# Optimization experiments

Hardware: AMD Instinct MI355X
Metric: run time of the kernel (lower is better)

Reference implementation:

```python
import jax, jax.numpy as jnp
import numpy as np

RADIUS = 12
SIGMA = 5.0
USM_LO, USM_HI = 0.0, 5.0
BEGIN = 0  # cfg.usm_begin_param


def _gauss_kernel_2d():
    x = jnp.arange(-RADIUS, RADIUS + 1, dtype=jnp.float32)
    k = jnp.exp(-0.5 * (x / SIGMA) ** 2)
    k = k / k.sum()
    return jnp.outer(k, k)  # [25, 25]


def setup_inputs() -> dict:
    key = jax.random.key(0)
    k1, k2 = jax.random.split(key)
    img = jax.random.uniform(k1, (16, 3, 512, 512), dtype=jnp.float32)
    features = jax.random.normal(k2, (16, 8), dtype=jnp.float32)
    return {"img": img, "features": features}


def reference(img, features):
    p = features[:, BEGIN:BEGIN + 1]                       # [B, 1]
    param = (jnp.tanh(p) * 0.5 + 0.5) * (USM_HI - USM_LO) + USM_LO

    # depthwise 25x25 gaussian blur with reflect padding
    kernel = jnp.broadcast_to(_gauss_kernel_2d(), (3, 1, 25, 25))  # OIHW, groups=3
    padded = jnp.pad(img, ((0, 0), (0, 0), (RADIUS, RADIUS), (RADIUS, RADIUS)),
                     mode='reflect')
    blurred = jax.lax.conv_general_dilated(
        padded, kernel, window_strides=(1, 1), padding='VALID',
        dimension_numbers=('NCHW', 'OIHW', 'NCHW'), feature_group_count=3)

    out = img + param.reshape(-1, 1, 1, 1) * (img - blurred)
    return out, param
```

## Files before the change

### kernel.cpp

```cpp
#include <hip/hip_runtime.h>
#include <hip/hip_fp16.h>


#define RADIUS 12
#define KS     25
#define TILE   64
#define PT     88
#define TA_LD  104
#define TB_LD  72
#define IMG_W  512
#define IMG_H  512
#define PLANE  (IMG_W * IMG_H)
#define NPLANE 48

#define N_STAGE (PT * 11)

__device__ __constant__ float GW[KS] = {
    0.00453456f, 0.00718308f, 0.01093238f, 0.01598625f, 0.02245983f,
    0.03031760f, 0.03931982f, 0.04899550f, 0.05865827f, 0.06747307f,
    0.07456928f, 0.07918039f, 0.08077993f, 0.07918039f, 0.07456928f,
    0.06747307f, 0.05865827f, 0.04899550f, 0.03931982f, 0.03031760f,
    0.02245983f, 0.01598625f, 0.01093238f, 0.00718308f, 0.00453456f
};

__device__ __forceinline__ int reflect512(int i) {
    i = (i < 0) ? -i : i;
    return (i >= 512) ? (1022 - i) : i;
}

typedef _Float16 h2_t __attribute__((ext_vector_type(2)));

__device__ __forceinline__ unsigned h2u(__half2 h) {
    union { __half2 h; unsigned u; } x; x.h = h; return x.u;
}
__device__ __forceinline__ __half2 u2h(unsigned u) {
    union { unsigned u; __half2 h; } x; x.u = u; return x.h;
}
__device__ __forceinline__ float u_lo(unsigned u) {
    return __half2float(__low2half(u2h(u)));
}
__device__ __forceinline__ float u_hi(unsigned u) {
    return __half2float(__high2half(u2h(u)));
}

#if __has_builtin(__builtin_amdgcn_fdot2)
__device__ __forceinline__ float fdot2u(unsigned a, unsigned b, float c) {
    union { unsigned u; h2_t h; } ua, ub;
    ua.u = a; ub.u = b;
    return __builtin_amdgcn_fdot2(ua.h, ub.h, c, false);
}
#else
__device__ __forceinline__ float fdot2u(unsigned a, unsigned b, float c) {
    return c + u_lo(a) * u_lo(b) + u_hi(a) * u_hi(b);
}
#endif

__global__ __launch_bounds__(256) void usm_fused_kernel(
    const float* __restrict__ img, const float* __restrict__ feat,
    float* __restrict__ out, float* __restrict__ out_param)
{
    __shared__ __half tileA[PT][TA_LD];
    __shared__ __half tmpB[PT][TB_LD];

    const int bid  = blockIdx.x + 8 * blockIdx.y + 64 * blockIdx.z;
    const int swz  = (bid & 7) * 384 + (bid >> 3);
    const int bx   = swz & 7;
    const int by   = (swz >> 3) & 7;
    const int zc   = swz >> 6;

    const int tid = threadIdx.x;
    const int tx0 = bx * TILE, ty0 = by * TILE;
    const int b   = zc / 3;
    const float* __restrict__ src = img + (size_t)zc * PLANE;

    float4 sva[4], svb[4];
#pragma unroll
    for (int it = 0; it < 4; ++it) {
        const int li = tid + it * 256;
        if (it < 3 || li < N_STAGE) {
            const int py = li / 11, s = li - py * 11;
            const int gy = reflect512(ty0 - RADIUS + py);
            const float* __restrict__ rowp = src + (size_t)gy * IMG_W;
            const int gx = tx0 - RADIUS + s * 8;
            if (gx >= 0 && gx + 7 <= 511) {
                sva[it] = *(const float4*)(rowp + gx);
                svb[it] = *(const float4*)(rowp + gx + 4);
            } else {
                float4 va, vb;
                va.x = rowp[reflect512(gx)];     va.y = rowp[reflect512(gx + 1)];
                va.z = rowp[reflect512(gx + 2)]; va.w = rowp[reflect512(gx + 3)];
                vb.x = rowp[reflect512(gx + 4)]; vb.y = rowp[reflect512(gx + 5)];
                vb.z = rowp[reflect512(gx + 6)]; vb.w = rowp[reflect512(gx + 7)];
                sva[it] = va; svb[it] = vb;
            }
        }
    }

    unsigned W2[12];
#pragma unroll
    for (int m = 0; m < 12; ++m)
        W2[m] = h2u(__floats2half2_rn(GW[2 * m], GW[2 * m + 1]));
    const unsigned WE = h2u(__floats2half2_rn(GW[24], 0.f));
    const unsigned WO = h2u(__floats2half2_rn(0.f, GW[24]));

    __half2 GWh2[KS];
#pragma unroll
    for (int k = 0; k < KS; ++k)
        GWh2[k] = __floats2half2_rn(GW[k], GW[k]);

    const float param = (tanhf(feat[b * 8]) * 0.5f + 0.5f) * 5.0f;

#pragma unroll
    for (int it = 0; it < 4; ++it) {
        const int li = tid + it * 256;
        if (it < 3 || li < N_STAGE) {
            const int py = li / 11, s = li - py * 11;
            uint4 pk;
            pk.x = h2u(__floats2half2_rn(sva[it].x, sva[it].y));
            pk.y = h2u(__floats2half2_rn(sva[it].z, sva[it].w));
            pk.z = h2u(__floats2half2_rn(svb[it].x, svb[it].y));
            pk.w = h2u(__floats2half2_rn(svb[it].z, svb[it].w));
            *(uint4*)&tileA[py][s * 8] = pk;
        }
    }
    __syncthreads();

#pragma unroll
    for (int it = 0; it < 3; ++it) {
        const int li = tid + it * 256;
        if (it < 2 || li < PT * (TILE / 8)) {
            const int py = li >> 3, g = li & 7;
            const uint4 qa = *(const uint4*)&tileA[py][g * 8];
            const uint4 qb = *(const uint4*)&tileA[py][g * 8 + 8];
            const uint4 qc = *(const uint4*)&tileA[py][g * 8 + 16];
            const uint4 qd = *(const uint4*)&tileA[py][g * 8 + 24];

            unsigned P[16] = { qa.x, qa.y, qa.z, qa.w, qb.x, qb.y, qb.z, qb.w,
                               qc.x, qc.y, qc.z, qc.w, qd.x, qd.y, qd.z, qd.w };
            unsigned S[15];
#pragma unroll
            for (int i = 0; i < 15; ++i)
                S[i] = __builtin_amdgcn_alignbit(P[i + 1], P[i], 16);

            float acc[8];
#pragma unroll
            for (int h = 0; h < 4; ++h) {
                float a = 0.f;
#pragma unroll
                for (int m = 0; m < 12; ++m) a = fdot2u(P[h + m], W2[m], a);
                acc[2 * h] = fdot2u(P[h + 12], WE, a);
            }
#pragma unroll
            for (int h = 0; h < 4; ++h) {
                float a = 0.f;
#pragma unroll
                for (int m = 0; m < 12; ++m) a = fdot2u(S[h + m], W2[m], a);
                acc[2 * h + 1] = fdot2u(P[h + 12], WO, a);
            }

            uint4 pk;
            pk.x = h2u(__floats2half2_rn(acc[0], acc[1]));
            pk.y = h2u(__floats2half2_rn(acc[2], acc[3]));
            pk.z = h2u(__floats2half2_rn(acc[4], acc[5]));
            pk.w = h2u(__floats2half2_rn(acc[6], acc[7]));
            *(uint4*)&tmpB[py][g * 8] = pk;
        }
    }
    __syncthreads();

    const int tx4 = (tid & 15) * 4, ry0 = (tid >> 4) * 4;

    __half2 aP0[4], aP1[4];
#pragma unroll
    for (int d = 0; d < 4; ++d) { aP0[d] = __half2(0, 0); aP1[d] = __half2(0, 0); }

#pragma unroll
    for (int k = 0; k < KS + 3; ++k) {
        const uint2 rd = *(const uint2*)&tmpB[ry0 + k][tx4];
        const __half2 p0 = u2h(rd.x), p1 = u2h(rd.y);
#pragma unroll
        for (int d = 0; d < 4; ++d) {
            const int kk = k - d;
            if (kk >= 0 && kk < KS) {
                aP0[d] = __hfma2(GWh2[kk], p0, aP0[d]);
                aP1[d] = __hfma2(GWh2[kk], p1, aP1[d]);
            }
        }
    }

    float* __restrict__ dst = out + (size_t)zc * PLANE;
#pragma unroll
    for (int d = 0; d < 4; ++d) {
        const int oy = ty0 + ry0 + d;
        const uint2 cv = *(const uint2*)&tileA[ry0 + d + RADIUS][tx4 + RADIUS];
        const float v0 = u_lo(cv.x), v1 = u_hi(cv.x), v2 = u_lo(cv.y), v3 = u_hi(cv.y);
        const float b0 = __half2float(__low2half(aP0[d])), b1 = __half2float(__high2half(aP0[d]));
        const float b2 = __half2float(__low2half(aP1[d])), b3 = __half2float(__high2half(aP1[d]));
        float4 o;
        o.x = v0 + param * (v0 - b0);
        o.y = v1 + param * (v1 - b1);
        o.z = v2 + param * (v2 - b2);
        o.w = v3 + param * (v3 - b3);
        *(float4*)(dst + (size_t)oy * IMG_W + tx0 + tx4) = o;
    }

    if (tid == 0 && bx == 0 && by == 0 && (zc - b * 3) == 0)
        out_param[b] = param;
}

extern "C" void kernel_launch(void* const* d_in, const int* in_sizes, int n_in,
                              void* d_out, int out_size, void* d_ws, size_t ws_size,
                              hipStream_t stream) {
    const float* img  = (const float*)d_in[0];
    const float* feat = (const float*)d_in[1];
    float* out       = (float*)d_out;
    float* out_param = (float*)d_out + (size_t)NPLANE * PLANE;

    usm_fused_kernel<<<dim3(8, 8, NPLANE), 256, 0, stream>>>(img, feat, out, out_param);
}
```

Baseline: 34.79 us.

## Offload part of horizontal blur pass to MFMA banded-matrix multiply

Computes the horizontal 25-tap blur for the first 48 tile rows with 16x16x32 f16 MFMA instructions against a banded Gaussian weight matrix built in registers. The remaining 40 rows stay on the existing fdot2 VALU path, so matrix and vector units can work concurrently. This reduces VALU pressure in the horizontal pass at the cost of extra registers and MFMAs that multiply many zero band entries. It also relies on the MFMA operand and result lane layouts being mapped correctly.

```diff
diff --git a/kernel.cpp b/kernel.cpp
--- a/kernel.cpp
+++ b/kernel.cpp
@@ -14,6 +14,7 @@
 #define NPLANE 48
 
 #define N_STAGE (PT * 11)
+#define N_H2    (40 * 8)
 
 __device__ __constant__ float GW[KS] = {
     0.00453456f, 0.00718308f, 0.01093238f, 0.01598625f, 0.02245983f,
@@ -29,6 +30,8 @@
 }
 
 typedef _Float16 h2_t __attribute__((ext_vector_type(2)));
+typedef _Float16 f16x8 __attribute__((ext_vector_type(8)));
+typedef float f32x4 __attribute__((ext_vector_type(4)));
 
 __device__ __forceinline__ unsigned h2u(__half2 h) {
     union { __half2 h; unsigned u; } x; x.h = h; return x.u;
@@ -72,6 +75,9 @@
     const int tx0 = bx * TILE, ty0 = by * TILE;
     const int b   = zc / 3;
     const float* __restrict__ src = img + (size_t)zc * PLANE;
+
+    const int lane = tid & 63, wid = tid >> 6;
+    const int r16 = lane & 15, kg = lane >> 4;
 
     float4 sva[4], svb[4];
 #pragma unroll
@@ -108,6 +114,16 @@
     for (int k = 0; k < KS; ++k)
         GWh2[k] = __floats2half2_rn(GW[k], GW[k]);
 
+    f16x8 X1, X2;
+#pragma unroll
+    for (int i = 0; i < 8; ++i) {
+        const int k = kg * 8 + i;
+        const int d1 = k - r16;
+        X1[i] = (d1 >= 0 && d1 < KS) ? (_Float16)GW[d1] : (_Float16)0.f;
+        const int d2 = 32 + k - r16;
+        X2[i] = (d2 < KS) ? (_Float16)GW[d2] : (_Float16)0.f;
+    }
+
     const float param = (tanhf(feat[b * 8]) * 0.5f + 0.5f) * 5.0f;
 
 #pragma unroll
@@ -125,11 +141,24 @@
     }
     __syncthreads();
 
-#pragma unroll
-    for (int it = 0; it < 3; ++it) {
+    f32x4 dmf0 = {0.f, 0.f, 0.f, 0.f}, dmf1 = dmf0, dmf2 = dmf0;
+#pragma unroll
+    for (int j = 0; j < 3; ++j) {
+        const int t = wid + j * 4;
+        const int py0 = (t >> 2) * 16, c0 = (t & 3) * 16;
+        const f16x8 Y1 = *(const f16x8*)&tileA[py0 + r16][c0 + kg * 8];
+        const f16x8 Y2 = *(const f16x8*)&tileA[py0 + r16][c0 + 32];
+        f32x4 d = {0.f, 0.f, 0.f, 0.f};
+        d = __builtin_amdgcn_mfma_f32_16x16x32_f16(X2, Y2, d, 0, 0, 0);
+        d = __builtin_amdgcn_mfma_f32_16x16x32_f16(X1, Y1, d, 0, 0, 0);
+        if (j == 0) dmf0 = d; else if (j == 1) dmf1 = d; else dmf2 = d;
+    }
+
+#pragma unroll
+    for (int it = 0; it < 2; ++it) {
         const int li = tid + it * 256;
-        if (it < 2 || li < PT * (TILE / 8)) {
-            const int py = li >> 3, g = li & 7;
+        if (it < 1 || li < N_H2) {
+            const int py = 48 + (li >> 3), g = li & 7;
             const uint4 qa = *(const uint4*)&tileA[py][g * 8];
             const uint4 qb = *(const uint4*)&tileA[py][g * 8 + 8];
             const uint4 qc = *(const uint4*)&tileA[py][g * 8 + 16];
@@ -165,6 +194,17 @@
             pk.w = h2u(__floats2half2_rn(acc[6], acc[7]));
             *(uint4*)&tmpB[py][g * 8] = pk;
         }
+    }
+
+#pragma unroll
+    for (int j = 0; j < 3; ++j) {
+        const int t = wid + j * 4;
+        const int py0 = (t >> 2) * 16, c0 = (t & 3) * 16;
+        const f32x4 d = (j == 0) ? dmf0 : (j == 1) ? dmf1 : dmf2;
+        uint2 w;
+        w.x = h2u(__floats2half2_rn(d[0], d[1]));
+        w.y = h2u(__floats2half2_rn(d[2], d[3]));
+        *(uint2*)&tmpB[py0 + r16][c0 + kg * 4] = w;
     }
     __syncthreads();
 
```

New measurement: 45.61 us. 31.1% more time.
